# Performance work log

Measured on AMD Instinct MI355X. Metric: run time of the kernel, lower is better.

The kernel has to match this reference:

```python
import jax, jax.numpy as jnp
import numpy as np

# Architecture constants (from RUMamba.__init__ hard-coded Mamba2 config)
D_MODEL = 512
D_STATE = 128
D_CONV = 4
EXPAND = 4
HEADDIM = 32
D_INNER = EXPAND * D_MODEL            # 2048
NHEADS = D_INNER // HEADDIM           # 64
CONV_DIM = D_INNER + 2 * D_STATE      # 2304 (ngroups=1)
D_IN_PROJ = 2 * D_INNER + 2 * D_STATE + NHEADS  # 4416
NUM_CLASS = 2513
BATCH = 4
SEQ = 16


def setup_inputs() -> dict:
    key = jax.random.key(0)
    ks = jax.random.split(key, 8)
    inputs = jax.random.normal(ks[0], (BATCH, SEQ, D_MODEL), jnp.float32)
    in_proj_w = jax.random.normal(ks[1], (D_IN_PROJ, D_MODEL), jnp.float32) * 0.02
    conv_w = jax.random.normal(ks[2], (CONV_DIM, D_CONV), jnp.float32) * 0.2
    conv_b = jnp.zeros((CONV_DIM,), jnp.float32)
    # dt_bias initialized so softplus(dt_bias) ~ U(0.001, 0.1), as in Mamba2
    dt = jax.random.uniform(ks[3], (NHEADS,), jnp.float32, 0.001, 0.1)
    dt_bias = dt + jnp.log(-jnp.expm1(-dt))
    A_log = jnp.log(jax.random.uniform(ks[4], (NHEADS,), jnp.float32, 1.0, 16.0))
    cls_w = jax.random.normal(ks[5], (NUM_CLASS, HEADDIM * D_STATE), jnp.float32) * 0.02
    cls_b = jnp.zeros((NUM_CLASS,), jnp.float32)
    return {"inputs": inputs, "in_proj_w": in_proj_w, "conv_w": conv_w,
            "conv_b": conv_b, "dt_bias": dt_bias, "A_log": A_log,
            "cls_w": cls_w, "cls_b": cls_b}


def reference(inputs, in_proj_w, conv_w, conv_b, dt_bias, A_log, cls_w, cls_b):
    # inputs: (B, S, D) -> (S, B, D) as in forward's permute(1,0,2)
    seq = jnp.transpose(inputs, (1, 0, 2))
    S, B, _ = seq.shape

    # Shared in_proj for both rolling and unrolling (same Mamba math on inputs[t]).
    zxbcdt = jnp.einsum('sbd,ed->sbe', seq, in_proj_w)        # (S,B,4416)
    xBC_raw = zxbcdt[..., D_INNER:D_INNER + CONV_DIM]          # (S,B,2304)
    dt = jax.nn.softplus(zxbcdt[..., -NHEADS:] + dt_bias)      # (S,B,H)
    A = -jnp.exp(A_log)                                        # (H,)
    dA = jnp.exp(dt * A)                                       # (S,B,H)

    # --- Rolling pass: one length-1 Mamba call per timestep, SSM state carried,
    # conv state NOT carried -> causal conv on a length-1 seq uses only last tap.
    xBC_r = jax.nn.silu(xBC_raw * conv_w[:, -1] + conv_b)      # (S,B,2304)
    x_r = xBC_r[..., :D_INNER].reshape(S, B, NHEADS, HEADDIM)  # (S,B,H,P)
    B_r = xBC_r[..., D_INNER:D_INNER + D_STATE]                # (S,B,N)
    dBx = dt[..., None, None] * B_r[:, :, None, None, :] * x_r[..., None]  # (S,B,H,P,N)

    def roll_step(h, inp):
        dA_t, dBx_t = inp
        h = dA_t[..., None, None] * h + dBx_t
        return h, h

    h0 = jnp.zeros((B, NHEADS, HEADDIM, D_STATE), seq.dtype)
    _, states = jax.lax.scan(roll_step, h0, (dA, dBx))         # (S,B,H,P,N)

    # --- Unrolling pass: for each t, feed inputs[t] repeated (S - t + 1) times
    # starting from states[t]. Constant input => conv output only depends on
    # min(step, d_conv-1) via cumulative sums of reversed conv taps.
    cw = jnp.cumsum(conv_w[:, ::-1], axis=1)                   # (2304,4)
    t_idx = jnp.arange(S)

    def unroll_step(h, k):
        w_k = cw[:, jnp.minimum(k, D_CONV - 1)]                # (2304,)
        xBC_k = jax.nn.silu(xBC_raw * w_k + conv_b)            # (S,B,2304)
        x_k = xBC_k[..., :D_INNER].reshape(S, B, NHEADS, HEADDIM)
        B_k = xBC_k[..., D_INNER:D_INNER + D_STATE]
        h_new = dA[..., None, None] * h + \
            dt[..., None, None] * B_k[:, :, None, None, :] * x_k[..., None]
        active = (k <= S - t_idx)[:, None, None, None, None]   # length S - t + 1
        return jnp.where(active, h_new, h), None

    h_fin, _ = jax.lax.scan(unroll_step, states, jnp.arange(S + 1))  # (S,B,H,P,N)

    # Head-reduce to headdim*d_state = 4096 features, classify.
    feats = jnp.mean(h_fin, axis=2).reshape(S, B, HEADDIM * D_STATE)
    feats = jnp.transpose(feats, (1, 0, 2))                    # (B,S,4096)
    y = feats @ cls_w.T + cls_b                                # (B,S,num_class)
    return y
```

## Files before the change

kernel.cpp:

```cpp
#include <hip/hip_runtime.h>
#include <math.h>

#define S_LEN    16
#define NTOK     64
#define DMODEL   512
#define XB_COLS  2176
#define ZX_COLS  2240
#define NCLASS   2513
#define FEATDIM  4096
#define PD_STRIDE 2516

typedef float f4v __attribute__((ext_vector_type(4)));

__global__ __launch_bounds__(256) void k_fpart(const float* __restrict__ X,
                                               const float* __restrict__ W,
                                               float* __restrict__ partF) {
    const int tid = threadIdx.x;
    const int kf  = blockIdx.y;
    const int jb  = blockIdx.x * 64;
    const int k0  = kf * 64;

    __shared__ float A[64][64];
    __shared__ float B[64][64];

    {
        const int t  = tid >> 2;
        const int kq = tid & 3;
        const int xrow = (t & 3) * 16 + (t >> 2);
        const int e = (jb + t < XB_COLS) ? (2048 + jb + t) : (2176 + jb + t);
#pragma unroll
        for (int q = 0; q < 4; ++q) {
            const int kk = kq * 16 + q * 4;
            const float4 va = *reinterpret_cast<const float4*>(
                X + (size_t)xrow * DMODEL + k0 + kk);
            A[kk + 0][t] = va.x; A[kk + 1][t] = va.y;
            A[kk + 2][t] = va.z; A[kk + 3][t] = va.w;
            const float4 vb = *reinterpret_cast<const float4*>(
                W + (size_t)e * DMODEL + k0 + kk);
            B[kk + 0][t] = vb.x; B[kk + 1][t] = vb.y;
            B[kk + 2][t] = vb.z; B[kk + 3][t] = vb.w;
        }
    }
    __syncthreads();

    const int ti = tid >> 4;
    const int ci = tid & 15;
    float acc[4][4] = {{0.f}};
#pragma unroll 4
    for (int k = 0; k < 64; ++k) {
        const f4v a = *reinterpret_cast<const f4v*>(&A[k][ti * 4]);
        const f4v b = *reinterpret_cast<const f4v*>(&B[k][ci * 4]);
#pragma unroll
        for (int j = 0; j < 4; ++j)
#pragma unroll
            for (int l = 0; l < 4; ++l)
                acc[j][l] += a[j] * b[l];
    }
#pragma unroll
    for (int l = 0; l < 4; ++l) {
        f4v s; s[0] = acc[0][l]; s[1] = acc[1][l]; s[2] = acc[2][l]; s[3] = acc[3][l];
        *reinterpret_cast<f4v*>(
            partF + ((size_t)kf * ZX_COLS + jb + ci * 4 + l) * 64 + ti * 4) = s;
    }
}

__global__ __launch_bounds__(256) void k_fepi(const float* __restrict__ partF, int KF,
                                              const float* __restrict__ conv_w,
                                              const float* __restrict__ conv_b,
                                              const float* __restrict__ dt_bias,
                                              const float* __restrict__ A_log,
                                              float* __restrict__ u,
                                              float* __restrict__ aArr,
                                              float* __restrict__ dArr) {
    const int lane = threadIdx.x & 63;
    const int j    = blockIdx.x * 4 + (threadIdx.x >> 6);
    float acc = 0.f;
    for (int kf = 0; kf < KF; ++kf)
        acc += partF[((size_t)kf * ZX_COLS + j) * 64 + lane];

    if (j < XB_COLS) {
        const float4 cwv = *reinterpret_cast<const float4*>(conv_w + j * 4);
        const float cb = conv_b[j];
        float wk[4];
        wk[0] = cwv.w;
        wk[1] = wk[0] + cwv.z;
        wk[2] = wk[1] + cwv.y;
        wk[3] = wk[2] + cwv.x;
#pragma unroll
        for (int k = 0; k < 4; ++k) {
            const float v = acc * wk[k] + cb;
            u[((size_t)k * NTOK + lane) * XB_COLS + j] = v / (1.f + expf(-v));
        }
    } else {
        const int h = j - XB_COLS;
        const float x = acc + dt_bias[h];
        const float d = (x > 20.f) ? x : log1pf(expf(x));
        dArr[lane * 64 + h] = d;
        aArr[lane * 64 + h] = expf(-d * expf(A_log[h]));
    }
}

__global__ __launch_bounds__(256) void k_feats(const float* __restrict__ u,
                                               const float* __restrict__ aArr,
                                               const float* __restrict__ dArr,
                                               float* __restrict__ feats) {
    const int t = blockIdx.x >> 2;
    const int b = blockIdx.x & 3;
    const int tid = threadIdx.x;
    const int K = 16 - t;
    const int nvec = t + 5;

    __shared__ float q[16][64];
    __shared__ float cu[4][64];
    __shared__ float WV[20][32];
    __shared__ float Bv[20][128];

    if (tid < 64) {
        const int h = tid;
        const int mt = t * 4 + b;
        const float a   = aArr[mt * 64 + h];
        const float dtv = dArr[mt * 64 + h];
        float p = 1.f;
        float c3 = 0.f, c2 = 0.f, c1 = 0.f, c0 = 0.f, cs = 0.f;
        for (int j = 0; j <= K + 1; ++j) {
            if (j <= K - 3) c3 += p;
            if (j == K - 2) c2 = p;
            if (j == K - 1) c1 = p;
            if (j == K)     c0 = p;
            if (j == K + 1) cs = p;
            p *= a;
        }
        cu[0][h] = dtv * c0;
        cu[1][h] = dtv * c1;
        cu[2][h] = dtv * c2;
        cu[3][h] = dtv * c3;
        float prod = 1.f;
        for (int s = t; s >= 0; --s) {
            const int ms = s * 4 + b;
            q[s][h] = cs * prod * dArr[ms * 64 + h];
            prod *= aArr[ms * 64 + h];
        }
    }
    __syncthreads();

    {
        const int i = tid & 31;
        const int vs = tid >> 5;
        for (int v = vs; v < nvec; v += 8) {
            float acc = 0.f;
            if (v <= t) {
                const float* base = u + (size_t)(v * 4 + b) * XB_COLS;
                for (int h = 0; h < 64; ++h) acc += q[v][h] * base[h * 32 + i];
            } else {
                const int kk = v - t - 1;
                const float* base = u + ((size_t)kk * NTOK + t * 4 + b) * XB_COLS;
                for (int h = 0; h < 64; ++h) acc += cu[kk][h] * base[h * 32 + i];
            }
            WV[v][i] = acc;
        }
    }
    for (int x = tid; x < nvec * 128; x += 256) {
        const int v = x >> 7, n = x & 127;
        size_t src;
        if (v <= t) src = (size_t)(v * 4 + b) * XB_COLS + 2048 + n;
        else        src = ((size_t)(v - t - 1) * NTOK + t * 4 + b) * XB_COLS + 2048 + n;
        Bv[v][n] = u[src];
    }
    __syncthreads();

    {
        const int i  = tid >> 3;
        const int n0 = (tid & 7) * 16;
        const int r  = b * 16 + t;
        float acc[16];
#pragma unroll
        for (int nn = 0; nn < 16; ++nn) acc[nn] = 0.f;
        for (int v = 0; v < nvec; ++v) {
            const float wvv = WV[v][i];
#pragma unroll
            for (int nn = 0; nn < 16; ++nn) acc[nn] += wvv * Bv[v][n0 + nn];
        }
        float* dst = feats + (size_t)r * FEATDIM + i * 128 + n0;
#pragma unroll
        for (int qq = 0; qq < 4; ++qq) {
            float4 v4;
            v4.x = acc[qq * 4 + 0] * (1.f / 64.f);
            v4.y = acc[qq * 4 + 1] * (1.f / 64.f);
            v4.z = acc[qq * 4 + 2] * (1.f / 64.f);
            v4.w = acc[qq * 4 + 3] * (1.f / 64.f);
            *reinterpret_cast<float4*>(dst + qq * 4) = v4;
        }
    }
}

__global__ __launch_bounds__(256) void k_cls(const float* __restrict__ feats,
                                             const float* __restrict__ Wc,
                                             float* __restrict__ partialD) {
    const int tid   = threadIdx.x;
    const int ks    = blockIdx.y;
    const int cbase = blockIdx.x * 128;
    const int chunk = FEATDIM / gridDim.y;
    const int nsub  = chunk / 64;

    __shared__ float A[64][64];
    __shared__ float B[64][128];

    const int ti = tid >> 4;
    const int ci = tid & 15;
    float acc[4][8] = {{0.f}};

    for (int st = 0; st < nsub; ++st) {
        const int k0 = ks * chunk + st * 64;
        __syncthreads();
        {
            const int t = tid >> 2, kq = tid & 3;
#pragma unroll
            for (int q = 0; q < 4; ++q) {
                const int kk = kq * 16 + q * 4;
                const float4 v = *reinterpret_cast<const float4*>(
                    feats + (size_t)t * FEATDIM + k0 + kk);
                A[kk + 0][t] = v.x; A[kk + 1][t] = v.y;
                A[kk + 2][t] = v.z; A[kk + 3][t] = v.w;
            }
#pragma unroll
            for (int h = 0; h < 2; ++h) {
                const int c = (tid >> 2) + h * 64;
                int cr = cbase + c; if (cr > NCLASS - 1) cr = NCLASS - 1;
#pragma unroll
                for (int q = 0; q < 4; ++q) {
                    const int kk = kq * 16 + q * 4;
                    const float4 v = *reinterpret_cast<const float4*>(
                        Wc + (size_t)cr * FEATDIM + k0 + kk);
                    B[kk + 0][c] = v.x; B[kk + 1][c] = v.y;
                    B[kk + 2][c] = v.z; B[kk + 3][c] = v.w;
                }
            }
        }
        __syncthreads();

#pragma unroll 2
        for (int k = 0; k < 64; ++k) {
            const f4v a  = *reinterpret_cast<const f4v*>(&A[k][ti * 4]);
            const f4v b0 = *reinterpret_cast<const f4v*>(&B[k][ci * 8]);
            const f4v b1 = *reinterpret_cast<const f4v*>(&B[k][ci * 8 + 4]);
#pragma unroll
            for (int j = 0; j < 4; ++j) {
#pragma unroll
                for (int l = 0; l < 4; ++l) {
                    acc[j][l]     += a[j] * b0[l];
                    acc[j][l + 4] += a[j] * b1[l];
                }
            }
        }
    }

    const size_t obase = (size_t)ks * (NTOK * PD_STRIDE);
    if (cbase + 127 < NCLASS) {
#pragma unroll
        for (int j = 0; j < 4; ++j) {
            f4v s0, s1;
#pragma unroll
            for (int l = 0; l < 4; ++l) { s0[l] = acc[j][l]; s1[l] = acc[j][l + 4]; }
            float* dst = partialD + obase + (size_t)(ti * 4 + j) * PD_STRIDE
                       + cbase + ci * 8;
            *reinterpret_cast<f4v*>(dst)     = s0;
            *reinterpret_cast<f4v*>(dst + 4) = s1;
        }
    } else {
#pragma unroll
        for (int j = 0; j < 4; ++j)
#pragma unroll
            for (int l = 0; l < 8; ++l) {
                const int c = cbase + ci * 8 + l;
                if (c < NCLASS)
                    partialD[obase + (size_t)(ti * 4 + j) * PD_STRIDE + c] = acc[j][l];
            }
    }
}

__global__ void k_out(const float* __restrict__ partialD, const float* __restrict__ cls_b,
                      float* __restrict__ out, int KC) {
    const int bx = blockIdx.x;
    const int r  = bx / 10;
    const int c  = (bx % 10) * 256 + threadIdx.x;
    if (c >= NCLASS) return;
    float s = cls_b[c];
    for (int ks = 0; ks < KC; ++ks)
        s += partialD[(size_t)ks * (NTOK * PD_STRIDE) + (size_t)r * PD_STRIDE + c];
    out[(size_t)r * NCLASS + c] = s;
}

extern "C" void kernel_launch(void* const* d_in, const int* in_sizes, int n_in,
                              void* d_out, int out_size, void* d_ws, size_t ws_size,
                              hipStream_t stream) {
    const float* inputs  = (const float*)d_in[0];
    const float* in_proj = (const float*)d_in[1];
    const float* conv_w  = (const float*)d_in[2];
    const float* conv_b  = (const float*)d_in[3];
    const float* dt_bias = (const float*)d_in[4];
    const float* A_log   = (const float*)d_in[5];
    const float* cls_w   = (const float*)d_in[6];
    const float* cls_b   = (const float*)d_in[7];
    float* out = (float*)d_out;

    float* ws = (float*)d_ws;
    float* aArr    = ws;
    float* dArr    = ws + 4096;
    float* feats   = ws + 8192;
    float* scr     = ws + 270336;
    float* u       = scr;
    float* partF   = scr + 557056;
    float* partialD = scr;

    int KC;
    if (ws_size >= 11386880u) KC = 16;
    else                      KC = 8;

    k_fpart <<<dim3(35, 8), 256, 0, stream>>>(inputs, in_proj, partF);
    k_fepi  <<<560, 256, 0, stream>>>(partF, 8, conv_w, conv_b, dt_bias, A_log,
                                      u, aArr, dArr);
    k_feats <<<64, 256, 0, stream>>>(u, aArr, dArr, feats);
    k_cls   <<<dim3(20, KC), 256, 0, stream>>>(feats, cls_w, partialD);
    k_out   <<<640, 256, 0, stream>>>(partialD, cls_b, out, KC);
}
```

Measured before the change: 68.07 us.

## Retile classifier GEMM to 64-thread blocks with 8x8 register tiles

The classifier split-K GEMM moves from 256-thread blocks covering 64x128 tiles to 64-thread blocks covering 64x64 tiles. Each thread now accumulates an 8x8 output tile instead of 4x8, and the grid doubles in the class dimension. Shared-memory fills are rewritten to transpose float4 loads in registers and store vectorised rows, removing the scalar transposed stores. This raises arithmetic intensity per LDS read and gives more blocks for the CUs to spread over, at the cost of higher register pressure and only one wavefront per block to hide latency.

```diff
diff --git a/kernel.cpp b/kernel.cpp
--- a/kernel.cpp
+++ b/kernel.cpp
@@ -193,88 +193,99 @@
     }
 }
 
-__global__ __launch_bounds__(256) void k_cls(const float* __restrict__ feats,
-                                             const float* __restrict__ Wc,
-                                             float* __restrict__ partialD) {
+__global__ __launch_bounds__(64) void k_cls(const float* __restrict__ feats,
+                                            const float* __restrict__ Wc,
+                                            float* __restrict__ partialD) {
     const int tid   = threadIdx.x;
     const int ks    = blockIdx.y;
-    const int cbase = blockIdx.x * 128;
+    const int cls0  = blockIdx.x * 64;
     const int chunk = FEATDIM / gridDim.y;
     const int nsub  = chunk / 64;
 
     __shared__ float A[64][64];
-    __shared__ float B[64][128];
-
-    const int ti = tid >> 4;
-    const int ci = tid & 15;
-    float acc[4][8] = {{0.f}};
+    __shared__ float B[64][64];
+
+    const int ti = tid >> 3;
+    const int ci = tid & 7;
+    const int sq = tid & 15;
+    const int sk = tid >> 4;
+
+    float acc[8][8] = {{0.f}};
 
     for (int st = 0; st < nsub; ++st) {
         const int k0 = ks * chunk + st * 64;
         __syncthreads();
-        {
-            const int t = tid >> 2, kq = tid & 3;
-#pragma unroll
-            for (int q = 0; q < 4; ++q) {
-                const int kk = kq * 16 + q * 4;
-                const float4 v = *reinterpret_cast<const float4*>(
-                    feats + (size_t)t * FEATDIM + k0 + kk);
-                A[kk + 0][t] = v.x; A[kk + 1][t] = v.y;
-                A[kk + 2][t] = v.z; A[kk + 3][t] = v.w;
-            }
-#pragma unroll
-            for (int h = 0; h < 2; ++h) {
-                const int c = (tid >> 2) + h * 64;
-                int cr = cbase + c; if (cr > NCLASS - 1) cr = NCLASS - 1;
-#pragma unroll
-                for (int q = 0; q < 4; ++q) {
-                    const int kk = kq * 16 + q * 4;
-                    const float4 v = *reinterpret_cast<const float4*>(
-                        Wc + (size_t)cr * FEATDIM + k0 + kk);
-                    B[kk + 0][c] = v.x; B[kk + 1][c] = v.y;
-                    B[kk + 2][c] = v.z; B[kk + 3][c] = v.w;
+#pragma unroll
+        for (int j = 0; j < 4; ++j) {
+            const int kslot = sk + j * 4;
+            float4 va[4];
+#pragma unroll
+            for (int r = 0; r < 4; ++r)
+                va[r] = *reinterpret_cast<const float4*>(
+                    feats + (size_t)(sq * 4 + r) * FEATDIM + k0 + kslot * 4);
+#pragma unroll
+            for (int s = 0; s < 4; ++s) {
+                f4v w; w[0] = (&va[0].x)[s]; w[1] = (&va[1].x)[s];
+                       w[2] = (&va[2].x)[s]; w[3] = (&va[3].x)[s];
+                *reinterpret_cast<f4v*>(&A[kslot * 4 + s][sq * 4]) = w;
+            }
+            float4 vb[4];
+#pragma unroll
+            for (int r = 0; r < 4; ++r) {
+                int cr = cls0 + sq * 4 + r; if (cr > NCLASS - 1) cr = NCLASS - 1;
+                vb[r] = *reinterpret_cast<const float4*>(
+                    Wc + (size_t)cr * FEATDIM + k0 + kslot * 4);
+            }
+#pragma unroll
+            for (int s = 0; s < 4; ++s) {
+                f4v w; w[0] = (&vb[0].x)[s]; w[1] = (&vb[1].x)[s];
+                       w[2] = (&vb[2].x)[s]; w[3] = (&vb[3].x)[s];
+                *reinterpret_cast<f4v*>(&B[kslot * 4 + s][sq * 4]) = w;
+            }
+        }
+        __syncthreads();
+
+#pragma unroll 8
+        for (int k = 0; k < 64; ++k) {
+            const f4v a0 = *reinterpret_cast<const f4v*>(&A[k][ti * 4]);
+            const f4v a1 = *reinterpret_cast<const f4v*>(&A[k][32 + ti * 4]);
+            const f4v b0 = *reinterpret_cast<const f4v*>(&B[k][ci * 4]);
+            const f4v b1 = *reinterpret_cast<const f4v*>(&B[k][32 + ci * 4]);
+#pragma unroll
+            for (int j = 0; j < 4; ++j) {
+#pragma unroll
+                for (int l = 0; l < 4; ++l) {
+                    acc[j][l]         += a0[j] * b0[l];
+                    acc[j][l + 4]     += a0[j] * b1[l];
+                    acc[j + 4][l]     += a1[j] * b0[l];
+                    acc[j + 4][l + 4] += a1[j] * b1[l];
                 }
             }
         }
-        __syncthreads();
-
-#pragma unroll 2
-        for (int k = 0; k < 64; ++k) {
-            const f4v a  = *reinterpret_cast<const f4v*>(&A[k][ti * 4]);
-            const f4v b0 = *reinterpret_cast<const f4v*>(&B[k][ci * 8]);
-            const f4v b1 = *reinterpret_cast<const f4v*>(&B[k][ci * 8 + 4]);
-#pragma unroll
-            for (int j = 0; j < 4; ++j) {
-#pragma unroll
-                for (int l = 0; l < 4; ++l) {
-                    acc[j][l]     += a[j] * b0[l];
-                    acc[j][l + 4] += a[j] * b1[l];
+    }
+
+    const size_t obase = (size_t)ks * (NTOK * PD_STRIDE);
+#pragma unroll
+    for (int ta = 0; ta < 2; ++ta) {
+#pragma unroll
+        for (int j = 0; j < 4; ++j) {
+            const int row = ta * 32 + ti * 4 + j;
+#pragma unroll
+            for (int cb = 0; cb < 2; ++cb) {
+                const int c = cls0 + cb * 32 + ci * 4;
+                f4v s;
+#pragma unroll
+                for (int l = 0; l < 4; ++l) s[l] = acc[ta * 4 + j][cb * 4 + l];
+                float* dst = partialD + obase + (size_t)row * PD_STRIDE + c;
+                if (c + 3 < NCLASS) {
+                    *reinterpret_cast<f4v*>(dst) = s;
+                } else {
+#pragma unroll
+                    for (int l = 0; l < 4; ++l)
+                        if (c + l < NCLASS) dst[l] = s[l];
                 }
             }
         }
-    }
-
-    const size_t obase = (size_t)ks * (NTOK * PD_STRIDE);
-    if (cbase + 127 < NCLASS) {
-#pragma unroll
-        for (int j = 0; j < 4; ++j) {
-            f4v s0, s1;
-#pragma unroll
-            for (int l = 0; l < 4; ++l) { s0[l] = acc[j][l]; s1[l] = acc[j][l + 4]; }
-            float* dst = partialD + obase + (size_t)(ti * 4 + j) * PD_STRIDE
-                       + cbase + ci * 8;
-            *reinterpret_cast<f4v*>(dst)     = s0;
-            *reinterpret_cast<f4v*>(dst + 4) = s1;
-        }
-    } else {
-#pragma unroll
-        for (int j = 0; j < 4; ++j)
-#pragma unroll
-            for (int l = 0; l < 8; ++l) {
-                const int c = cbase + ci * 8 + l;
-                if (c < NCLASS)
-                    partialD[obase + (size_t)(ti * 4 + j) * PD_STRIDE + c] = acc[j][l];
-            }
     }
 }
 
@@ -320,6 +331,6 @@
     k_fepi  <<<560, 256, 0, stream>>>(partF, 8, conv_w, conv_b, dt_bias, A_log,
                                       u, aArr, dArr);
     k_feats <<<64, 256, 0, stream>>>(u, aArr, dArr, feats);
-    k_cls   <<<dim3(20, KC), 256, 0, stream>>>(feats, cls_w, partialD);
+    k_cls   <<<dim3(40, KC), 64, 0, stream>>>(feats, cls_w, partialD);
     k_out   <<<640, 256, 0, stream>>>(partialD, cls_b, out, KC);
 }
```

Result: slower. 69.91 us (+2.7%).
